# Optimization experiments

Hardware: AMD Instinct MI355X
Metric: run time of the kernel (lower is better)

## Reference

```python
import jax, jax.numpy as jnp
import numpy as np
import math

HIDDEN = 768
HEADS = 12
HEAD_DIM = HIDDEN // HEADS
B, T = 2, 2048


def setup_inputs() -> dict:
    key = jax.random.key(0)
    k1, k2, k3, k4, k5 = jax.random.split(key, 5)
    s = 0.02
    return {
        "x": jax.random.normal(k1, (B, T, HIDDEN), dtype=jnp.float32),
        "mask": jnp.ones((B, T), dtype=jnp.int32),
        "w_qkv": jax.random.normal(k2, (3 * HIDDEN, HIDDEN), dtype=jnp.float32) * s,
        "b_qkv": jnp.zeros((3 * HIDDEN,), dtype=jnp.float32),
        "w_out": jax.random.normal(k3, (HIDDEN, HIDDEN), dtype=jnp.float32) * s,
        "b_out": jnp.zeros((HIDDEN,), dtype=jnp.float32),
    }


def reference(x, mask, w_qkv, b_qkv, w_out, b_out):
    Bv, Tv, C = x.shape
    # torch Linear: y = x @ W.T + b
    qkv = jnp.einsum('btc,oc->bto', x, w_qkv) + b_qkv  # [B,T,3C]
    q, k, v = jnp.split(qkv, 3, axis=-1)
    def to_heads(t):
        return t.reshape(Bv, Tv, HEADS, HEAD_DIM).transpose(0, 2, 1, 3)  # [B,H,T,D]
    q, k, v = to_heads(q), to_heads(k), to_heads(v)
    scale = 1.0 / math.sqrt(HEAD_DIM)
    scores = jnp.einsum('bhqd,bhkd->bhqk', q, k) * scale  # [B,H,T,T]
    m = (mask[:, None, None, :] != 0)  # broadcast over heads and query dim
    scores = jnp.where(m, scores, -jnp.inf)
    probs = jax.nn.softmax(scores, axis=-1)
    # dropout is identity in eval mode
    ctx = jnp.einsum('bhqk,bhkd->bhqd', probs, v)  # [B,H,T,D]
    ctx = ctx.transpose(0, 2, 1, 3).reshape(Bv, Tv, C)
    return jnp.einsum('btc,oc->bto', ctx, w_out) + b_out
```

## Files before the change

### kernel.cpp

```cpp
#include <hip/hip_runtime.h>
#include <hip/hip_bf16.h>


typedef __bf16 bf16;
typedef __attribute__((ext_vector_type(4))) __bf16 bf16x4;
typedef __attribute__((ext_vector_type(8))) __bf16 bf16x8;
typedef __attribute__((ext_vector_type(4))) float f32x4;
typedef __attribute__((ext_vector_type(16))) float f32x16;
typedef __attribute__((ext_vector_type(4))) unsigned u32x4;

#define MFMA16(a, b, c) __builtin_amdgcn_mfma_f32_16x16x32_bf16((a), (b), (c), 0, 0, 0)
#define MFMA32(a, b, c) __builtin_amdgcn_mfma_f32_32x32x16_bf16((a), (b), (c), 0, 0, 0)

static constexpr int BB = 2;
static constexpr int TT = 2048;
static constexpr int CC = 768;
static constexpr int HH = 12;
static constexpr int DD = 64;

union U8 { u32x4 u; bf16x8 b; };

__device__ inline void gload16(const bf16* g, bf16* l) {
  __builtin_amdgcn_global_load_lds((const __attribute__((address_space(1))) void*)g,
                                   (__attribute__((address_space(3))) void*)l, 16, 0, 0);
}

__global__ __launch_bounds__(256) void cvt_all(const float* __restrict__ x,
                                               const float* __restrict__ wq,
                                               const float* __restrict__ wo,
                                               bf16* __restrict__ xb,
                                               bf16* __restrict__ wqb,
                                               bf16* __restrict__ wob) {
  const int CX = BB * TT * CC / 8, CQ = 3 * CC * CC / 8;
  int idx = blockIdx.x * 256 + threadIdx.x;
  const float* s;
  bf16* d;
  int off;
  if (idx < CX) { s = x; d = xb; off = idx; }
  else if (idx < CX + CQ) { s = wq; d = wqb; off = idx - CX; }
  else { s = wo; d = wob; off = idx - CX - CQ; }
  const float4* p = (const float4*)(s + (size_t)off * 8);
  float4 a = p[0], b = p[1];
  bf16x8 r;
  r[0] = (bf16)a.x; r[1] = (bf16)a.y; r[2] = (bf16)a.z; r[3] = (bf16)a.w;
  r[4] = (bf16)b.x; r[5] = (bf16)b.y; r[6] = (bf16)b.z; r[7] = (bf16)b.w;
  *(bf16x8*)(d + (size_t)off * 8) = r;
}

template <typename OT>
__global__ __launch_bounds__(256) void gemm_bt_bf16(const bf16* __restrict__ A,
                                                    const bf16* __restrict__ Bw,
                                                    const float* __restrict__ bias,
                                                    OT* __restrict__ Cmat,
                                                    int M, int N, int K,
                                                    float qs, int qcols) {
  __shared__ bf16 As[128 * 64];
  __shared__ bf16 Bs[128 * 64];
  const int tid = threadIdx.x;
  const int m0 = blockIdx.y * 128, n0 = blockIdx.x * 128;
  const int lane = tid & 63, w = tid >> 6;
  const int wm = (w >> 1) * 64, wn = (w & 1) * 64;
  const int lr = lane & 15;
  const int g4 = lane >> 4;
  const int srow8 = lane >> 3;
  const int scs = ((lane & 7) ^ srow8) * 8;
  f32x4 acc[4][4] = {};
  for (int k0 = 0; k0 < K; k0 += 64) {
    __syncthreads();
#pragma unroll
    for (int s = 0; s < 4; s++) {
      const int rowl = w * 32 + s * 8;
      gload16(A  + (size_t)(m0 + rowl + srow8) * K + k0 + scs, &As[rowl * 64]);
      gload16(Bw + (size_t)(n0 + rowl + srow8) * K + k0 + scs, &Bs[rowl * 64]);
    }
    __syncthreads();
#pragma unroll
    for (int ks = 0; ks < 2; ks++) {
      bf16x8 a[4], b[4];
#pragma unroll
      for (int i = 0; i < 4; i++)
        a[i] = *(const bf16x8*)&As[(wm + i * 16 + lr) * 64 + (((ks * 4 + g4) ^ (lr & 7)) * 8)];
#pragma unroll
      for (int j = 0; j < 4; j++)
        b[j] = *(const bf16x8*)&Bs[(wn + j * 16 + lr) * 64 + (((ks * 4 + g4) ^ (lr & 7)) * 8)];
#pragma unroll
      for (int i = 0; i < 4; i++)
#pragma unroll
        for (int j = 0; j < 4; j++)
          acc[i][j] = MFMA16(a[i], b[j], acc[i][j]);
    }
  }
#pragma unroll
  for (int i = 0; i < 4; i++) {
    const int rbase = m0 + wm + i * 16 + (lane >> 4) * 4;
#pragma unroll
    for (int j = 0; j < 4; j++) {
      const int cidx = n0 + wn + j * 16 + lr;
      const float bv = bias[cidx];
      const float sc = (cidx < qcols) ? qs : 1.0f;
#pragma unroll
      for (int r = 0; r < 4; r++) {
        float v = (acc[i][j][r] + bv) * sc;
        Cmat[(size_t)(rbase + r) * N + cidx] = (OT)v;
      }
    }
  }
}

template <int NS>
__global__ __launch_bounds__(256, 4) void attn_fwd(const bf16* __restrict__ qkv,
                                                   const int* __restrict__ mask,
                                                   bf16* __restrict__ po,
                                                   float* __restrict__ ml,
                                                   bf16* __restrict__ ctx) {
  __shared__ bf16 Ks[2][32 * 64];
  __shared__ bf16 Vt[2][64 * 32];
  const int tid = threadIdx.x, lane = tid & 63, w = tid >> 6;
  const int ln31 = lane & 31, hi = lane >> 5;
  const int cpx = 48 * NS;
  const int bid = blockIdx.x;
  const int wg = (bid & 7) * cpx + (bid >> 3);
  const int qb = wg & 15;
  const int t2 = wg >> 4;
  const int s = t2 % NS;
  const int bh = t2 / NS;
  const int h = bh % HH, b = bh / HH;
  const int q = qb * 128 + w * 32 + ln31;
  const size_t rs = 3 * CC;
  const float NEG = -1.0e30f;
  const int kt0 = s * (TT / NS), kt1 = kt0 + TT / NS;

  bf16x8 qreg[4];
  {
    const bf16* qp = qkv + (size_t)(b * TT + q) * rs + h * DD + hi * 8;
#pragma unroll
    for (int ds = 0; ds < 4; ds++) qreg[ds] = *(const bf16x8*)(qp + ds * 16);
  }

  const bf16* kbase = qkv + (size_t)(b * TT) * rs + CC + h * DD;
  const bf16* vbase = qkv + (size_t)(b * TT) * rs + 2 * CC + h * DD;

  const int kkey = w * 8 + (lane >> 3);
  const int kcs = (lane & 7) ^ (kkey & 7) ^ (kkey >> 3);
  auto stage_k = [&](int buf, int kt) {
    gload16(kbase + (size_t)(kt + kkey) * rs + kcs * 8, &Ks[buf][w * 512]);
  };

  const int vkey = w * 8 + (lane >> 3);
  const int vd0 = (lane & 7) * 8;
  const int vpar = vkey & 1;
  const int vkp = vkey >> 1;
  bf16x8 vreg;
  int mv;
  auto load_v = [&](int kt) {
    vreg = *(const bf16x8*)(vbase + (size_t)(kt + vkey) * rs + vd0);
    mv = mask[b * TT + kt + ln31];
  };
  auto vt_put = [&](int buf, int d, int kp, unsigned val) {
    const int cp = (kp >> 2) ^ (d & 3) ^ ((d >> 2) & 3);
    *(unsigned*)&Vt[buf][d * 32 + cp * 8 + (kp & 3) * 2] = val;
  };
  auto write_v = [&](int buf) {
    U8 uu; uu.b = vreg;
    const u32x4 wv = uu.u;
    unsigned x0 = vpar ? wv[0] : wv[2];
    unsigned x1 = vpar ? wv[1] : wv[3];
    unsigned r0 = __shfl_xor(x0, 8);
    unsigned r1 = __shfl_xor(x1, 8);
    unsigned a0 = vpar ? r0 : wv[0];
    unsigned a1 = vpar ? r1 : wv[1];
    unsigned b0 = vpar ? wv[2] : r0;
    unsigned b1 = vpar ? wv[3] : r1;
    const int dbase = vd0 + vpar * 4;
    vt_put(buf, dbase + 0, vkp, (a0 & 0xffffu) | (b0 << 16));
    vt_put(buf, dbase + 1, vkp, (a0 >> 16) | (b0 & 0xffff0000u));
    vt_put(buf, dbase + 2, vkp, (a1 & 0xffffu) | (b1 << 16));
    vt_put(buf, dbase + 3, vkp, (a1 >> 16) | (b1 & 0xffff0000u));
  };

  stage_k(0, kt0);
  load_v(kt0);
  write_v(0);
  __syncthreads();
  int mvc = mv;

  f32x16 oacc0 = {}, oacc1 = {};
  float m = NEG, l = 0.f;
  const int swr = (ln31 & 7) ^ (ln31 >> 3);
  const int vsw = (ln31 & 3) ^ ((ln31 >> 2) & 3);

  int cur = 0;
  for (int kt = kt0; kt < kt1; kt += 32, cur ^= 1) {
    const bool more = kt + 32 < kt1;
    if (more) { stage_k(cur ^ 1, kt + 32); load_v(kt + 32); }

    f32x16 sacc = {};
#pragma unroll
    for (int ds = 0; ds < 4; ds++) {
      bf16x8 kf = *(const bf16x8*)&Ks[cur][ln31 * 64 + ((ds * 2 + hi) ^ swr) * 8];
      sacc = MFMA32(kf, qreg[ds], sacc);
    }

    const unsigned mw = (unsigned)__ballot(mvc != 0);
    if (mw != 0xffffffffu) {
      const unsigned mwh = mw >> (4 * hi);
#pragma unroll
      for (int r = 0; r < 16; r++) {
        const int key = (r & 3) + 8 * (r >> 2);
        if (!((mwh >> key) & 1)) sacc[r] = NEG;
      }
    }

    float mx = sacc[0];
#pragma unroll
    for (int r = 1; r < 16; r++) mx = fmaxf(mx, sacc[r]);
    mx = fmaxf(mx, __shfl_xor(mx, 32));
    if (!__all(mx - m <= 8.f)) {
      const float al = exp2f(m - mx);
      l *= al;
#pragma unroll
      for (int r = 0; r < 16; r++) { oacc0[r] *= al; oacc1[r] *= al; }
      m = mx;
    }
    float p[16], rsum = 0.f;
#pragma unroll
    for (int r = 0; r < 16; r++) { p[r] = exp2f(sacc[r] - m); rsum += p[r]; }
    rsum += __shfl_xor(rsum, 32);
    l += rsum;

    unsigned pk[8];
#pragma unroll
    for (int i = 0; i < 8; i++)
      asm("v_cvt_pk_bf16_f32 %0, %1, %2" : "=v"(pk[i]) : "v"(p[2 * i]), "v"(p[2 * i + 1]));
    asm volatile("v_permlane32_swap_b32 %0, %1" : "+v"(pk[0]), "+v"(pk[2]));
    asm volatile("v_permlane32_swap_b32 %0, %1" : "+v"(pk[1]), "+v"(pk[3]));
    asm volatile("v_permlane32_swap_b32 %0, %1" : "+v"(pk[4]), "+v"(pk[6]));
    asm volatile("v_permlane32_swap_b32 %0, %1" : "+v"(pk[5]), "+v"(pk[7]));

#pragma unroll
    for (int ks = 0; ks < 2; ks++) {
      U8 uu;
      uu.u = (u32x4){pk[ks * 4 + 0], pk[ks * 4 + 1], pk[ks * 4 + 2], pk[ks * 4 + 3]};
      const bf16x8 pb = uu.b;
      const int cph = ((ks * 2 + hi) ^ vsw) * 8;
      bf16x8 vf0 = *(const bf16x8*)&Vt[cur][ln31 * 32 + cph];
      oacc0 = MFMA32(vf0, pb, oacc0);
      bf16x8 vf1 = *(const bf16x8*)&Vt[cur][(32 + ln31) * 32 + cph];
      oacc1 = MFMA32(vf1, pb, oacc1);
    }

    if (more) write_v(cur ^ 1);
    __syncthreads();
    mvc = mv;
  }

  const float invl = l > 0.f ? 1.0f / l : 0.f;
  const size_t gr = (size_t)(b * TT + q);
  bf16* obase = (NS == 1) ? (ctx + gr * CC + h * DD)
                          : (po + (size_t)s * (BB * TT * CC) + gr * CC + h * DD);
#pragma unroll
  for (int g = 0; g < 4; g++) {
    bf16x4 o0, o1;
#pragma unroll
    for (int j = 0; j < 4; j++) {
      o0[j] = (bf16)(oacc0[4 * g + j] * invl);
      o1[j] = (bf16)(oacc1[4 * g + j] * invl);
    }
    *(bf16x4*)(obase + 8 * g + 4 * hi) = o0;
    *(bf16x4*)(obase + 32 + 8 * g + 4 * hi) = o1;
  }
  if (NS > 1 && hi == 0) {
    float2 v2 = {m, l};
    *(float2*)&ml[(((size_t)s * (BB * TT) + gr) * HH + h) * 2] = v2;
  }
}

template <int NS>
__global__ __launch_bounds__(256) void combine(const bf16* __restrict__ po,
                                               const float* __restrict__ ml,
                                               bf16* __restrict__ ctx) {
  const int idx = blockIdx.x * 256 + threadIdx.x;
  const int row = idx / 96;
  const int rem = idx - row * 96;
  const int h = rem >> 3, d8 = rem & 7;
  float ms[NS], ls[NS];
  float M = -1.0e30f;
#pragma unroll
  for (int s = 0; s < NS; s++) {
    const float2 p2 = *(const float2*)&ml[(((size_t)s * (BB * TT) + row) * HH + h) * 2];
    ms[s] = p2.x; ls[s] = p2.y;
    M = fmaxf(M, p2.x);
  }
  float wgt[NS], wsum = 0.f;
#pragma unroll
  for (int s = 0; s < NS; s++) { wgt[s] = ls[s] * exp2f(ms[s] - M); wsum += wgt[s]; }
  const float inv = wsum > 0.f ? 1.0f / wsum : 0.f;
  float acc[8] = {};
#pragma unroll
  for (int s = 0; s < NS; s++) {
    const float ws = wgt[s] * inv;
    const bf16x8 v = *(const bf16x8*)&po[(size_t)s * (BB * TT * CC) + (size_t)row * CC + h * 64 + d8 * 8];
#pragma unroll
    for (int j = 0; j < 8; j++) acc[j] += ws * (float)v[j];
  }
  bf16x8 o;
#pragma unroll
  for (int j = 0; j < 8; j++) o[j] = (bf16)acc[j];
  *(bf16x8*)&ctx[(size_t)row * CC + h * 64 + d8 * 8] = o;
}

extern "C" void kernel_launch(void* const* d_in, const int* in_sizes, int n_in,
                              void* d_out, int out_size, void* d_ws, size_t ws_size,
                              hipStream_t stream) {
  const float* x     = (const float*)d_in[0];
  const int*   mask  = (const int*)d_in[1];
  const float* w_qkv = (const float*)d_in[2];
  const float* b_qkv = (const float*)d_in[3];
  const float* w_out = (const float*)d_in[4];
  const float* b_out = (const float*)d_in[5];
  float* out = (float*)d_out;

  const int M = BB * TT;
  bf16* qkv = (bf16*)d_ws;
  bf16* xb  = qkv + (size_t)M * 3 * CC;
  bf16* ctx = xb;
  bf16* wob = xb + (size_t)M * CC;
  bf16* wqb = wob + (size_t)CC * CC;
  const size_t PO_OFF = (size_t)((M * 3 * CC) + (M * CC) + (CC * CC)) * 2;
  const size_t PER_SPLIT = (size_t)M * CC * 2 + (size_t)M * HH * 2 * 4;

  int NS = 1;
  if (ws_size >= PO_OFF + 4 * PER_SPLIT) NS = 4;
  else if (ws_size >= PO_OFF + 2 * PER_SPLIT) NS = 2;

  bf16* po = (bf16*)((char*)d_ws + PO_OFF);
  float* ml = (float*)((char*)d_ws + PO_OFF + (size_t)NS * M * CC * 2);

  const int nchunks = (BB * TT * CC + 3 * CC * CC + CC * CC) / 8;
  cvt_all<<<nchunks / 256, 256, 0, stream>>>(x, w_qkv, w_out, xb, wqb, wob);
  gemm_bt_bf16<bf16><<<dim3(3 * CC / 128, M / 128), 256, 0, stream>>>(
      xb, wqb, b_qkv, qkv, M, 3 * CC, CC, 0.125f * 1.44269504f, CC);
  if (NS == 4) {
    attn_fwd<4><<<dim3(384 * 4), 256, 0, stream>>>(qkv, mask, po, ml, ctx);
    combine<4><<<dim3(M * HH * 8 / 256), 256, 0, stream>>>(po, ml, ctx);
  } else if (NS == 2) {
    attn_fwd<2><<<dim3(384 * 2), 256, 0, stream>>>(qkv, mask, po, ml, ctx);
    combine<2><<<dim3(M * HH * 8 / 256), 256, 0, stream>>>(po, ml, ctx);
  } else {
    attn_fwd<1><<<dim3(384), 256, 0, stream>>>(qkv, mask, po, ml, ctx);
  }
  gemm_bt_bf16<float><<<dim3(CC / 128, M / 128), 256, 0, stream>>>(
      ctx, wob, b_out, out, M, CC, CC, 1.0f, 0);
}
```

Measured before the change: 114.8 us.

## Double attention key tile to 64 keys per iteration with new LDS swizzles

The attention loop now processes 64 keys per iteration instead of 32, with two QK score accumulators and four PV MFMA steps per tile. The K and V LDS staging, transpose shuffles and XOR swizzles are reworked for 64-wide rows. s_setprio is raised around the MFMA blocks. This halves the number of barriers and loop overheads per key and gives the scheduler more independent MFMA work, at the cost of more LDS and registers, which may lower occupancy.

```diff
diff --git a/kernel.cpp b/kernel.cpp
--- a/kernel.cpp
+++ b/kernel.cpp
@@ -113,8 +113,8 @@
                                                    bf16* __restrict__ po,
                                                    float* __restrict__ ml,
                                                    bf16* __restrict__ ctx) {
-  __shared__ bf16 Ks[2][32 * 64];
-  __shared__ bf16 Vt[2][64 * 32];
+  __shared__ bf16 Ks[2][64 * 64];
+  __shared__ bf16 Vt[2][64 * 64];
   const int tid = threadIdx.x, lane = tid & 63, w = tid >> 6;
   const int ln31 = lane & 31, hi = lane >> 5;
   const int cpx = 48 * NS;
@@ -140,42 +140,50 @@
   const bf16* kbase = qkv + (size_t)(b * TT) * rs + CC + h * DD;
   const bf16* vbase = qkv + (size_t)(b * TT) * rs + 2 * CC + h * DD;
 
-  const int kkey = w * 8 + (lane >> 3);
-  const int kcs = (lane & 7) ^ (kkey & 7) ^ (kkey >> 3);
+  const int krow = lane >> 3;
+  const int klc0 = ((lane & 7) ^ (w & 7)) * 8;
+  const int klc1 = ((lane & 7) ^ ((w + 4) & 7)) * 8;
   auto stage_k = [&](int buf, int kt) {
-    gload16(kbase + (size_t)(kt + kkey) * rs + kcs * 8, &Ks[buf][w * 512]);
+    gload16(kbase + (size_t)(kt + w * 8 + krow) * rs + klc0, &Ks[buf][(w * 8) * 64]);
+    gload16(kbase + (size_t)(kt + 32 + w * 8 + krow) * rs + klc1, &Ks[buf][(32 + w * 8) * 64]);
   };
 
-  const int vkey = w * 8 + (lane >> 3);
-  const int vd0 = (lane & 7) * 8;
+  const int vkey = tid >> 2;
+  const int vd0 = (tid & 3) * 16;
   const int vpar = vkey & 1;
   const int vkp = vkey >> 1;
-  bf16x8 vreg;
+  bf16x8 vr0, vr1;
   int mv;
   auto load_v = [&](int kt) {
-    vreg = *(const bf16x8*)(vbase + (size_t)(kt + vkey) * rs + vd0);
-    mv = mask[b * TT + kt + ln31];
+    const bf16* vp = vbase + (size_t)(kt + vkey) * rs + vd0;
+    vr0 = ((const bf16x8*)vp)[0];
+    vr1 = ((const bf16x8*)vp)[1];
+    mv = mask[b * TT + kt + lane];
   };
-  auto vt_put = [&](int buf, int d, int kp, unsigned val) {
-    const int cp = (kp >> 2) ^ (d & 3) ^ ((d >> 2) & 3);
-    *(unsigned*)&Vt[buf][d * 32 + cp * 8 + (kp & 3) * 2] = val;
+  auto vt_put = [&](int buf, int d, unsigned val) {
+    *(unsigned*)&Vt[buf][d * 64 + (((vkp >> 2) ^ ((d >> 3) & 7)) * 8) + (vkp & 3) * 2] = val;
   };
   auto write_v = [&](int buf) {
-    U8 uu; uu.b = vreg;
-    const u32x4 wv = uu.u;
-    unsigned x0 = vpar ? wv[0] : wv[2];
-    unsigned x1 = vpar ? wv[1] : wv[3];
-    unsigned r0 = __shfl_xor(x0, 8);
-    unsigned r1 = __shfl_xor(x1, 8);
-    unsigned a0 = vpar ? r0 : wv[0];
-    unsigned a1 = vpar ? r1 : wv[1];
-    unsigned b0 = vpar ? wv[2] : r0;
-    unsigned b1 = vpar ? wv[3] : r1;
-    const int dbase = vd0 + vpar * 4;
-    vt_put(buf, dbase + 0, vkp, (a0 & 0xffffu) | (b0 << 16));
-    vt_put(buf, dbase + 1, vkp, (a0 >> 16) | (b0 & 0xffff0000u));
-    vt_put(buf, dbase + 2, vkp, (a1 & 0xffffu) | (b1 << 16));
-    vt_put(buf, dbase + 3, vkp, (a1 >> 16) | (b1 & 0xffff0000u));
+    U8 ua, ub; ua.b = vr0; ub.b = vr1;
+    unsigned w0 = ua.u[0], w1 = ua.u[1], w2 = ua.u[2], w3 = ua.u[3];
+    unsigned w4 = ub.u[0], w5 = ub.u[1], w6 = ub.u[2], w7 = ub.u[3];
+    unsigned x0 = vpar ? w0 : w4, x1 = vpar ? w1 : w5;
+    unsigned x2 = vpar ? w2 : w6, x3 = vpar ? w3 : w7;
+    unsigned r0 = __shfl_xor(x0, 4), r1 = __shfl_xor(x1, 4);
+    unsigned r2 = __shfl_xor(x2, 4), r3 = __shfl_xor(x3, 4);
+    unsigned a0 = vpar ? r0 : w0, a1 = vpar ? r1 : w1;
+    unsigned a2 = vpar ? r2 : w2, a3 = vpar ? r3 : w3;
+    unsigned b0 = vpar ? w4 : r0, b1 = vpar ? w5 : r1;
+    unsigned b2 = vpar ? w6 : r2, b3 = vpar ? w7 : r3;
+    const int dbase = vd0 + vpar * 8;
+    vt_put(buf, dbase + 0, (a0 & 0xffffu) | (b0 << 16));
+    vt_put(buf, dbase + 1, (a0 >> 16) | (b0 & 0xffff0000u));
+    vt_put(buf, dbase + 2, (a1 & 0xffffu) | (b1 << 16));
+    vt_put(buf, dbase + 3, (a1 >> 16) | (b1 & 0xffff0000u));
+    vt_put(buf, dbase + 4, (a2 & 0xffffu) | (b2 << 16));
+    vt_put(buf, dbase + 5, (a2 >> 16) | (b2 & 0xffff0000u));
+    vt_put(buf, dbase + 6, (a3 & 0xffffu) | (b3 << 16));
+    vt_put(buf, dbase + 7, (a3 >> 16) | (b3 & 0xffff0000u));
   };
 
   stage_k(0, kt0);
@@ -186,34 +194,39 @@
 
   f32x16 oacc0 = {}, oacc1 = {};
   float m = NEG, l = 0.f;
-  const int swr = (ln31 & 7) ^ (ln31 >> 3);
-  const int vsw = (ln31 & 3) ^ ((ln31 >> 2) & 3);
+  const int rsw0 = (ln31 >> 3) & 7;
+  const int rsw1 = ((32 + ln31) >> 3) & 7;
 
   int cur = 0;
-  for (int kt = kt0; kt < kt1; kt += 32, cur ^= 1) {
-    const bool more = kt + 32 < kt1;
-    if (more) { stage_k(cur ^ 1, kt + 32); load_v(kt + 32); }
-
-    f32x16 sacc = {};
+  for (int kt = kt0; kt < kt1; kt += 64, cur ^= 1) {
+    const bool more = kt + 64 < kt1;
+    if (more) { stage_k(cur ^ 1, kt + 64); load_v(kt + 64); }
+
+    f32x16 sa = {}, sb = {};
+    __builtin_amdgcn_s_setprio(1);
 #pragma unroll
     for (int ds = 0; ds < 4; ds++) {
-      bf16x8 kf = *(const bf16x8*)&Ks[cur][ln31 * 64 + ((ds * 2 + hi) ^ swr) * 8];
-      sacc = MFMA32(kf, qreg[ds], sacc);
-    }
-
-    const unsigned mw = (unsigned)__ballot(mvc != 0);
-    if (mw != 0xffffffffu) {
-      const unsigned mwh = mw >> (4 * hi);
+      const int c0 = ds * 2 + hi;
+      bf16x8 kfa = *(const bf16x8*)&Ks[cur][ln31 * 64 + ((c0 ^ rsw0) * 8)];
+      sa = MFMA32(kfa, qreg[ds], sa);
+      bf16x8 kfb = *(const bf16x8*)&Ks[cur][(32 + ln31) * 64 + ((c0 ^ rsw1) * 8)];
+      sb = MFMA32(kfb, qreg[ds], sb);
+    }
+    __builtin_amdgcn_s_setprio(0);
+
+    const unsigned long long bm = __ballot(mvc != 0);
+    if (bm != ~0ull) {
 #pragma unroll
       for (int r = 0; r < 16; r++) {
-        const int key = (r & 3) + 8 * (r >> 2);
-        if (!((mwh >> key) & 1)) sacc[r] = NEG;
+        const int key = (r & 3) + 8 * (r >> 2) + 4 * hi;
+        if (!((bm >> key) & 1)) sa[r] = NEG;
+        if (!((bm >> (key + 32)) & 1)) sb[r] = NEG;
       }
     }
 
-    float mx = sacc[0];
-#pragma unroll
-    for (int r = 1; r < 16; r++) mx = fmaxf(mx, sacc[r]);
+    float mx = fmaxf(sa[0], sb[0]);
+#pragma unroll
+    for (int r = 1; r < 16; r++) mx = fmaxf(mx, fmaxf(sa[r], sb[r]));
     mx = fmaxf(mx, __shfl_xor(mx, 32));
     if (!__all(mx - m <= 8.f)) {
       const float al = exp2f(m - mx);
@@ -222,32 +235,43 @@
       for (int r = 0; r < 16; r++) { oacc0[r] *= al; oacc1[r] *= al; }
       m = mx;
     }
-    float p[16], rsum = 0.f;
-#pragma unroll
-    for (int r = 0; r < 16; r++) { p[r] = exp2f(sacc[r] - m); rsum += p[r]; }
+    float rsum = 0.f;
+#pragma unroll
+    for (int r = 0; r < 16; r++) {
+      sa[r] = exp2f(sa[r] - m); rsum += sa[r];
+      sb[r] = exp2f(sb[r] - m); rsum += sb[r];
+    }
     rsum += __shfl_xor(rsum, 32);
     l += rsum;
 
-    unsigned pk[8];
-#pragma unroll
-    for (int i = 0; i < 8; i++)
-      asm("v_cvt_pk_bf16_f32 %0, %1, %2" : "=v"(pk[i]) : "v"(p[2 * i]), "v"(p[2 * i + 1]));
+    unsigned pk[16];
+#pragma unroll
+    for (int i = 0; i < 8; i++) {
+      asm("v_cvt_pk_bf16_f32 %0, %1, %2" : "=v"(pk[i]) : "v"(sa[2 * i]), "v"(sa[2 * i + 1]));
+      asm("v_cvt_pk_bf16_f32 %0, %1, %2" : "=v"(pk[8 + i]) : "v"(sb[2 * i]), "v"(sb[2 * i + 1]));
+    }
     asm volatile("v_permlane32_swap_b32 %0, %1" : "+v"(pk[0]), "+v"(pk[2]));
     asm volatile("v_permlane32_swap_b32 %0, %1" : "+v"(pk[1]), "+v"(pk[3]));
     asm volatile("v_permlane32_swap_b32 %0, %1" : "+v"(pk[4]), "+v"(pk[6]));
     asm volatile("v_permlane32_swap_b32 %0, %1" : "+v"(pk[5]), "+v"(pk[7]));
-
-#pragma unroll
-    for (int ks = 0; ks < 2; ks++) {
+    asm volatile("v_permlane32_swap_b32 %0, %1" : "+v"(pk[8]), "+v"(pk[10]));
+    asm volatile("v_permlane32_swap_b32 %0, %1" : "+v"(pk[9]), "+v"(pk[11]));
+    asm volatile("v_permlane32_swap_b32 %0, %1" : "+v"(pk[12]), "+v"(pk[14]));
+    asm volatile("v_permlane32_swap_b32 %0, %1" : "+v"(pk[13]), "+v"(pk[15]));
+
+    __builtin_amdgcn_s_setprio(1);
+#pragma unroll
+    for (int ks = 0; ks < 4; ks++) {
       U8 uu;
       uu.u = (u32x4){pk[ks * 4 + 0], pk[ks * 4 + 1], pk[ks * 4 + 2], pk[ks * 4 + 3]};
       const bf16x8 pb = uu.b;
-      const int cph = ((ks * 2 + hi) ^ vsw) * 8;
-      bf16x8 vf0 = *(const bf16x8*)&Vt[cur][ln31 * 32 + cph];
+      const int c0 = ks * 2 + hi;
+      bf16x8 vf0 = *(const bf16x8*)&Vt[cur][ln31 * 64 + ((c0 ^ rsw0) * 8)];
       oacc0 = MFMA32(vf0, pb, oacc0);
-      bf16x8 vf1 = *(const bf16x8*)&Vt[cur][(32 + ln31) * 32 + cph];
+      bf16x8 vf1 = *(const bf16x8*)&Vt[cur][(32 + ln31) * 64 + ((c0 ^ rsw1) * 8)];
       oacc1 = MFMA32(vf1, pb, oacc1);
     }
+    __builtin_amdgcn_s_setprio(0);
 
     if (more) write_v(cur ^ 1);
     __syncthreads();
```

Result: slower. 128.7 us (+12.1%).

## Use 64-key attention tiles, precomputed mask bitwords, and MFMA priority hints

Applied to the files above, without the earlier changes.

The attention kernel now processes 64 keys per iteration instead of 32, doubling the K and V shared-memory tiles and halving the number of barriers per key range. The second V half-tile is loaded and transposed in the middle of the iteration to overlap with compute. Mask loads and per-iteration ballots are replaced by 32-bit mask words built once by an extra block in the conversion kernel. s_setprio hints are placed around the MFMA sections. Larger LDS use (32KB per block) may reduce occupancy, and register pressure rises.

```diff
diff --git a/kernel.cpp b/kernel.cpp
--- a/kernel.cpp
+++ b/kernel.cpp
@@ -28,9 +28,21 @@
 __global__ __launch_bounds__(256) void cvt_all(const float* __restrict__ x,
                                                const float* __restrict__ wq,
                                                const float* __restrict__ wo,
+                                               const int* __restrict__ mask,
                                                bf16* __restrict__ xb,
                                                bf16* __restrict__ wqb,
-                                               bf16* __restrict__ wob) {
+                                               bf16* __restrict__ wob,
+                                               unsigned* __restrict__ mbits) {
+  if (blockIdx.x == gridDim.x - 1) {
+    const int i = threadIdx.x;
+    if (i < BB * TT / 32) {
+      unsigned wrd = 0;
+#pragma unroll
+      for (int j = 0; j < 32; j++) wrd |= (mask[i * 32 + j] != 0 ? 1u : 0u) << j;
+      mbits[i] = wrd;
+    }
+    return;
+  }
   const int CX = BB * TT * CC / 8, CQ = 3 * CC * CC / 8;
   int idx = blockIdx.x * 256 + threadIdx.x;
   const float* s;
@@ -109,12 +121,12 @@
 
 template <int NS>
 __global__ __launch_bounds__(256, 4) void attn_fwd(const bf16* __restrict__ qkv,
-                                                   const int* __restrict__ mask,
+                                                   const unsigned* __restrict__ mbits,
                                                    bf16* __restrict__ po,
                                                    float* __restrict__ ml,
                                                    bf16* __restrict__ ctx) {
-  __shared__ bf16 Ks[2][32 * 64];
-  __shared__ bf16 Vt[2][64 * 32];
+  __shared__ bf16 Ks[2][64 * 64];
+  __shared__ bf16 Vt[2][64 * 64];
   const int tid = threadIdx.x, lane = tid & 63, w = tid >> 6;
   const int ln31 = lane & 31, hi = lane >> 5;
   const int cpx = 48 * NS;
@@ -128,7 +140,8 @@
   const int q = qb * 128 + w * 32 + ln31;
   const size_t rs = 3 * CC;
   const float NEG = -1.0e30f;
-  const int kt0 = s * (TT / NS), kt1 = kt0 + TT / NS;
+  const int kt0 = s * (TT / NS);
+  const int NT = (TT / NS) / 64;
 
   bf16x8 qreg[4];
   {
@@ -139,28 +152,26 @@
 
   const bf16* kbase = qkv + (size_t)(b * TT) * rs + CC + h * DD;
   const bf16* vbase = qkv + (size_t)(b * TT) * rs + 2 * CC + h * DD;
-
-  const int kkey = w * 8 + (lane >> 3);
-  const int kcs = (lane & 7) ^ (kkey & 7) ^ (kkey >> 3);
-  auto stage_k = [&](int buf, int kt) {
-    gload16(kbase + (size_t)(kt + kkey) * rs + kcs * 8, &Ks[buf][w * 512]);
-  };
+  const size_t stride = (size_t)64 * rs;
+
+  const int krow = lane >> 3;
+  const int kcsA = ((lane & 7) ^ krow ^ w) * 8;
+  const int kcsB = ((lane & 7) ^ krow ^ (w + 4)) * 8;
+  const bf16* kptA = kbase + (size_t)(kt0 + w * 8 + krow) * rs + kcsA;
+  const bf16* kptB = kbase + (size_t)(kt0 + 32 + w * 8 + krow) * rs + kcsB;
 
   const int vkey = w * 8 + (lane >> 3);
   const int vd0 = (lane & 7) * 8;
   const int vpar = vkey & 1;
   const int vkp = vkey >> 1;
+  const bf16* vptr = vbase + (size_t)(kt0 + vkey) * rs + vd0;
+
   bf16x8 vreg;
-  int mv;
-  auto load_v = [&](int kt) {
-    vreg = *(const bf16x8*)(vbase + (size_t)(kt + vkey) * rs + vd0);
-    mv = mask[b * TT + kt + ln31];
+  auto vt_put = [&](int buf, int d, int p, unsigned val) {
+    const int cp = (p >> 2) ^ (d & 7) ^ ((d >> 3) & 7);
+    *(unsigned*)&Vt[buf][d * 64 + cp * 8 + (p & 3) * 2] = val;
   };
-  auto vt_put = [&](int buf, int d, int kp, unsigned val) {
-    const int cp = (kp >> 2) ^ (d & 3) ^ ((d >> 2) & 3);
-    *(unsigned*)&Vt[buf][d * 32 + cp * 8 + (kp & 3) * 2] = val;
-  };
-  auto write_v = [&](int buf) {
+  auto write_v = [&](int buf, int pbase) {
     U8 uu; uu.b = vreg;
     const u32x4 wv = uu.u;
     unsigned x0 = vpar ? wv[0] : wv[2];
@@ -172,86 +183,117 @@
     unsigned b0 = vpar ? wv[2] : r0;
     unsigned b1 = vpar ? wv[3] : r1;
     const int dbase = vd0 + vpar * 4;
-    vt_put(buf, dbase + 0, vkp, (a0 & 0xffffu) | (b0 << 16));
-    vt_put(buf, dbase + 1, vkp, (a0 >> 16) | (b0 & 0xffff0000u));
-    vt_put(buf, dbase + 2, vkp, (a1 & 0xffffu) | (b1 << 16));
-    vt_put(buf, dbase + 3, vkp, (a1 >> 16) | (b1 & 0xffff0000u));
+    const int p = pbase + vkp;
+    vt_put(buf, dbase + 0, p, (a0 & 0xffffu) | (b0 << 16));
+    vt_put(buf, dbase + 1, p, (a0 >> 16) | (b0 & 0xffff0000u));
+    vt_put(buf, dbase + 2, p, (a1 & 0xffffu) | (b1 << 16));
+    vt_put(buf, dbase + 3, p, (a1 >> 16) | (b1 & 0xffff0000u));
   };
 
-  stage_k(0, kt0);
-  load_v(kt0);
-  write_v(0);
+  gload16(kptA, &Ks[0][(w * 8) * 64]);
+  gload16(kptB, &Ks[0][(32 + w * 8) * 64]);
+  vreg = *(const bf16x8*)vptr;
+  write_v(0, 0);
+  vreg = *(const bf16x8*)(vptr + (size_t)32 * rs);
+  write_v(0, 16);
+  kptA += stride; kptB += stride; vptr += stride;
   __syncthreads();
-  int mvc = mv;
 
   f32x16 oacc0 = {}, oacc1 = {};
   float m = NEG, l = 0.f;
-  const int swr = (ln31 & 7) ^ (ln31 >> 3);
-  const int vsw = (ln31 & 3) ^ ((ln31 >> 2) & 3);
+  const int swrA = (ln31 & 7) ^ (ln31 >> 3);
+  const int swrB = swrA ^ 4;
+  int mbase = (b * TT + kt0) >> 5;
 
   int cur = 0;
-  for (int kt = kt0; kt < kt1; kt += 32, cur ^= 1) {
-    const bool more = kt + 32 < kt1;
-    if (more) { stage_k(cur ^ 1, kt + 32); load_v(kt + 32); }
-
-    f32x16 sacc = {};
-#pragma unroll
-    for (int ds = 0; ds < 4; ds++) {
-      bf16x8 kf = *(const bf16x8*)&Ks[cur][ln31 * 64 + ((ds * 2 + hi) ^ swr) * 8];
-      sacc = MFMA32(kf, qreg[ds], sacc);
-    }
-
-    const unsigned mw = (unsigned)__ballot(mvc != 0);
-    if (mw != 0xffffffffu) {
-      const unsigned mwh = mw >> (4 * hi);
-#pragma unroll
-      for (int r = 0; r < 16; r++) {
-        const int key = (r & 3) + 8 * (r >> 2);
-        if (!((mwh >> key) & 1)) sacc[r] = NEG;
-      }
-    }
-
-    float mx = sacc[0];
-#pragma unroll
-    for (int r = 1; r < 16; r++) mx = fmaxf(mx, sacc[r]);
-    mx = fmaxf(mx, __shfl_xor(mx, 32));
-    if (!__all(mx - m <= 8.f)) {
-      const float al = exp2f(m - mx);
-      l *= al;
-#pragma unroll
-      for (int r = 0; r < 16; r++) { oacc0[r] *= al; oacc1[r] *= al; }
-      m = mx;
-    }
-    float p[16], rsum = 0.f;
-#pragma unroll
-    for (int r = 0; r < 16; r++) { p[r] = exp2f(sacc[r] - m); rsum += p[r]; }
+  for (int it = 0; it < NT; ++it, cur ^= 1) {
+    const bool more = (it + 1 < NT);
+    if (more) {
+      gload16(kptA, &Ks[cur ^ 1][(w * 8) * 64]);
+      gload16(kptB, &Ks[cur ^ 1][(32 + w * 8) * 64]);
+      vreg = *(const bf16x8*)vptr;
+      kptA += stride; kptB += stride;
+    }
+    const unsigned mwA = mbits[mbase], mwB = mbits[mbase + 1];
+    mbase += 2;
+
+    float rsum = 0.f;
+    unsigned pk[8];
+
+#pragma unroll
+    for (int half = 0; half < 2; half++) {
+      f32x16 sacc = {};
+      const int rbase = half * 32;
+      const int swr = half ? swrB : swrA;
+      __builtin_amdgcn_s_setprio(1);
+#pragma unroll
+      for (int ds = 0; ds < 4; ds++) {
+        bf16x8 kf = *(const bf16x8*)&Ks[cur][(rbase + ln31) * 64 + (((ds * 2 + hi) ^ swr) * 8)];
+        sacc = MFMA32(kf, qreg[ds], sacc);
+      }
+      __builtin_amdgcn_s_setprio(0);
+
+      const unsigned mw = half ? mwB : mwA;
+      if (mw != 0xffffffffu) {
+#pragma unroll
+        for (int r = 0; r < 16; r++) {
+          const int key = (r & 3) + 8 * (r >> 2) + 4 * hi;
+          if (!((mw >> key) & 1)) sacc[r] = NEG;
+        }
+      }
+
+      float t0 = fmaxf(fmaxf(sacc[0], sacc[1]), sacc[2]);
+      float t1 = fmaxf(fmaxf(sacc[3], sacc[4]), sacc[5]);
+      float t2 = fmaxf(fmaxf(sacc[6], sacc[7]), sacc[8]);
+      float t3 = fmaxf(fmaxf(sacc[9], sacc[10]), sacc[11]);
+      float t4 = fmaxf(fmaxf(sacc[12], sacc[13]), sacc[14]);
+      float mx = fmaxf(fmaxf(fmaxf(t0, t1), fmaxf(t2, t3)), fmaxf(t4, sacc[15]));
+      mx = fmaxf(mx, __shfl_xor(mx, 32));
+      if (!__all(mx - m <= 8.f)) {
+        const float al = exp2f(m - mx);
+        l *= al;
+#pragma unroll
+        for (int r = 0; r < 16; r++) { oacc0[r] *= al; oacc1[r] *= al; }
+        m = mx;
+      }
+#pragma unroll
+      for (int r = 0; r < 16; r++) { sacc[r] = exp2f(sacc[r] - m); rsum += sacc[r]; }
+
+#pragma unroll
+      for (int i = 0; i < 8; i++)
+        asm("v_cvt_pk_bf16_f32 %0, %1, %2" : "=v"(pk[i]) : "v"(sacc[2 * i]), "v"(sacc[2 * i + 1]));
+      asm volatile("v_permlane32_swap_b32 %0, %1" : "+v"(pk[0]), "+v"(pk[2]));
+      asm volatile("v_permlane32_swap_b32 %0, %1" : "+v"(pk[1]), "+v"(pk[3]));
+      asm volatile("v_permlane32_swap_b32 %0, %1" : "+v"(pk[4]), "+v"(pk[6]));
+      asm volatile("v_permlane32_swap_b32 %0, %1" : "+v"(pk[5]), "+v"(pk[7]));
+
+      if (more) {
+        if (half == 0) {
+          write_v(cur ^ 1, 0);
+          vreg = *(const bf16x8*)(vptr + (size_t)32 * rs);
+        }
+      }
+
+      __builtin_amdgcn_s_setprio(1);
+#pragma unroll
+      for (int ks = 0; ks < 2; ks++) {
+        U8 uu;
+        uu.u = (u32x4){pk[ks * 4 + 0], pk[ks * 4 + 1], pk[ks * 4 + 2], pk[ks * 4 + 3]};
+        const bf16x8 pb = uu.b;
+        const int cg = (half * 2 + ks) * 2 + hi;
+        bf16x8 vf0 = *(const bf16x8*)&Vt[cur][ln31 * 64 + ((cg ^ swrA) * 8)];
+        oacc0 = MFMA32(vf0, pb, oacc0);
+        bf16x8 vf1 = *(const bf16x8*)&Vt[cur][(32 + ln31) * 64 + ((cg ^ swrB) * 8)];
+        oacc1 = MFMA32(vf1, pb, oacc1);
+      }
+      __builtin_amdgcn_s_setprio(0);
+    }
+
     rsum += __shfl_xor(rsum, 32);
     l += rsum;
 
-    unsigned pk[8];
-#pragma unroll
-    for (int i = 0; i < 8; i++)
-      asm("v_cvt_pk_bf16_f32 %0, %1, %2" : "=v"(pk[i]) : "v"(p[2 * i]), "v"(p[2 * i + 1]));
-    asm volatile("v_permlane32_swap_b32 %0, %1" : "+v"(pk[0]), "+v"(pk[2]));
-    asm volatile("v_permlane32_swap_b32 %0, %1" : "+v"(pk[1]), "+v"(pk[3]));
-    asm volatile("v_permlane32_swap_b32 %0, %1" : "+v"(pk[4]), "+v"(pk[6]));
-    asm volatile("v_permlane32_swap_b32 %0, %1" : "+v"(pk[5]), "+v"(pk[7]));
-
-#pragma unroll
-    for (int ks = 0; ks < 2; ks++) {
-      U8 uu;
-      uu.u = (u32x4){pk[ks * 4 + 0], pk[ks * 4 + 1], pk[ks * 4 + 2], pk[ks * 4 + 3]};
-      const bf16x8 pb = uu.b;
-      const int cph = ((ks * 2 + hi) ^ vsw) * 8;
-      bf16x8 vf0 = *(const bf16x8*)&Vt[cur][ln31 * 32 + cph];
-      oacc0 = MFMA32(vf0, pb, oacc0);
-      bf16x8 vf1 = *(const bf16x8*)&Vt[cur][(32 + ln31) * 32 + cph];
-      oacc1 = MFMA32(vf1, pb, oacc1);
-    }
-
-    if (more) write_v(cur ^ 1);
+    if (more) { write_v(cur ^ 1, 16); vptr += stride; }
     __syncthreads();
-    mvc = mv;
   }
 
   const float invl = l > 0.f ? 1.0f / l : 0.f;
@@ -330,24 +372,25 @@
   const size_t PER_SPLIT = (size_t)M * CC * 2 + (size_t)M * HH * 2 * 4;
 
   int NS = 1;
-  if (ws_size >= PO_OFF + 4 * PER_SPLIT) NS = 4;
-  else if (ws_size >= PO_OFF + 2 * PER_SPLIT) NS = 2;
+  if (ws_size >= PO_OFF + 4 * PER_SPLIT + 512) NS = 4;
+  else if (ws_size >= PO_OFF + 2 * PER_SPLIT + 512) NS = 2;
 
   bf16* po = (bf16*)((char*)d_ws + PO_OFF);
   float* ml = (float*)((char*)d_ws + PO_OFF + (size_t)NS * M * CC * 2);
+  unsigned* mbits = (unsigned*)((char*)d_ws + PO_OFF + (size_t)NS * PER_SPLIT);
 
   const int nchunks = (BB * TT * CC + 3 * CC * CC + CC * CC) / 8;
-  cvt_all<<<nchunks / 256, 256, 0, stream>>>(x, w_qkv, w_out, xb, wqb, wob);
+  cvt_all<<<nchunks / 256 + 1, 256, 0, stream>>>(x, w_qkv, w_out, mask, xb, wqb, wob, mbits);
   gemm_bt_bf16<bf16><<<dim3(3 * CC / 128, M / 128), 256, 0, stream>>>(
       xb, wqb, b_qkv, qkv, M, 3 * CC, CC, 0.125f * 1.44269504f, CC);
   if (NS == 4) {
-    attn_fwd<4><<<dim3(384 * 4), 256, 0, stream>>>(qkv, mask, po, ml, ctx);
+    attn_fwd<4><<<dim3(384 * 4), 256, 0, stream>>>(qkv, mbits, po, ml, ctx);
     combine<4><<<dim3(M * HH * 8 / 256), 256, 0, stream>>>(po, ml, ctx);
   } else if (NS == 2) {
-    attn_fwd<2><<<dim3(384 * 2), 256, 0, stream>>>(qkv, mask, po, ml, ctx);
+    attn_fwd<2><<<dim3(384 * 2), 256, 0, stream>>>(qkv, mbits, po, ml, ctx);
     combine<2><<<dim3(M * HH * 8 / 256), 256, 0, stream>>>(po, ml, ctx);
   } else {
-    attn_fwd<1><<<dim3(384), 256, 0, stream>>>(qkv, mask, po, ml, ctx);
+    attn_fwd<1><<<dim3(384), 256, 0, stream>>>(qkv, mbits, po, ml, ctx);
   }
   gemm_bt_bf16<float><<<dim3(CC / 128, M / 128), 256, 0, stream>>>(
       ctx, wob, b_out, out, M, CC, CC, 1.0f, 0);
```

Measured after the change: 124.9 us. 8.7% more time.
